# Kernel tuning notes

Hardware: AMD Instinct MI355X
Metric: run time of the kernel (lower is better)

## Reference

```python
import jax, jax.numpy as jnp
import numpy as np

D_MODEL = 1024
H = 16
D_K = D_MODEL // H


def setup_inputs() -> dict:
    key = jax.random.key(0)
    ks = jax.random.split(key, 9)
    B, S = 4, 2048
    s = 1.0 / np.sqrt(D_MODEL)
    return {
        "query": jax.random.normal(ks[0], (B, S, D_MODEL), jnp.float32),
        "key_": jax.random.normal(ks[1], (B, S, D_MODEL), jnp.float32),
        "value": jax.random.normal(ks[2], (B, S, D_MODEL), jnp.float32),
        "Wq": jax.random.normal(ks[3], (D_MODEL, D_MODEL), jnp.float32) * s,
        "bq": jnp.zeros((D_MODEL,), jnp.float32),
        "Wk": jax.random.normal(ks[4], (D_MODEL, D_MODEL), jnp.float32) * s,
        "bk": jnp.zeros((D_MODEL,), jnp.float32),
        "Wv": jax.random.normal(ks[5], (D_MODEL, D_MODEL), jnp.float32) * s,
        "bv": jnp.zeros((D_MODEL,), jnp.float32),
    }


def reference(query, key_, value, Wq, bq, Wk, bk, Wv, bv):
    B, S, _ = query.shape
    # separate Q/K/V projections (torch Linear: x @ W.T + b)
    q = (query @ Wq.T + bq).reshape(B, S, H, D_K).transpose(0, 2, 1, 3)  # [B,H,S,Dk]
    k = (key_ @ Wk.T + bk).reshape(B, S, H, D_K).transpose(0, 2, 1, 3)
    v = (value @ Wv.T + bv).reshape(B, S, H, D_K).transpose(0, 2, 1, 3)
    # naive scaled dot-product attention (full [B,H,S,S] scores)
    scores = jnp.einsum("bhqd,bhkd->bhqk", q, k) / jnp.sqrt(jnp.float32(D_K))
    attn = jax.nn.softmax(scores, axis=-1)
    out = jnp.einsum("bhqk,bhkd->bhqd", attn, v)  # [B,H,S,Dk]
    # merge heads; NOTE: original forward never applies self.wo
    return out.transpose(0, 2, 1, 3).reshape(B, S, D_MODEL)
```

## Files before the change

kernel.cpp:

```cpp
#include <hip/hip_runtime.h>
#include <math.h>

#define DEVI __device__ __forceinline__

typedef short bf16x8 __attribute__((ext_vector_type(8)));
typedef float f32x4 __attribute__((ext_vector_type(4)));
typedef float f32x16 __attribute__((ext_vector_type(16)));
typedef unsigned short u16x8 __attribute__((ext_vector_type(8)));
typedef unsigned short u16x4 __attribute__((ext_vector_type(4)));
typedef unsigned int u32x2 __attribute__((ext_vector_type(2)));
typedef int i32x4 __attribute__((ext_vector_type(4)));

static constexpr int S_LEN = 2048;
static constexpr int DMODEL = 1024;
static constexpr int NH = 16;
static constexpr int DK = 64;

DEVI unsigned short f2bf(float f) {
  unsigned int u = __builtin_bit_cast(unsigned int, f);
  u = u + 0x7fffu + ((u >> 16) & 1u);
  return (unsigned short)(u >> 16);
}
DEVI unsigned cvtpk(float lo, float hi) {
  unsigned d;
  asm("v_cvt_pk_bf16_f32 %0, %1, %2" : "=v"(d) : "v"(lo), "v"(hi));
  return d;
}
DEVI float bitf(unsigned u) { return __builtin_bit_cast(float, u); }
DEVI unsigned bitu(float f) { return __builtin_bit_cast(unsigned, f); }

#if __has_builtin(__builtin_amdgcn_exp2f)
DEVI float fexp2(float x) { return __builtin_amdgcn_exp2f(x); }
#else
DEVI float fexp2(float x) { return __expf(x * 0.69314718055994531f); }
#endif

typedef __attribute__((address_space(3))) unsigned int lds_u32;
typedef __attribute__((address_space(1))) const unsigned int glb_u32;

DEVI void gload16(const void* g, void* lds) {
  __builtin_amdgcn_global_load_lds((glb_u32*)reinterpret_cast<uintptr_t>(g),
                                   (lds_u32*)reinterpret_cast<uintptr_t>(lds),
                                   16, 0, 0);
}

__global__ __launch_bounds__(256) void cvt_f32_bf16(const float* __restrict__ in,
                                                    unsigned short* __restrict__ out,
                                                    int n8) {
  int i = blockIdx.x * 256 + threadIdx.x;
  if (i >= n8) return;
  const float4* p = (const float4*)in + (size_t)i * 2;
  float4 a = p[0], b = p[1];
  u16x8 o;
  o[0] = f2bf(a.x); o[1] = f2bf(a.y); o[2] = f2bf(a.z); o[3] = f2bf(a.w);
  o[4] = f2bf(b.x); o[5] = f2bf(b.y); o[6] = f2bf(b.z); o[7] = f2bf(b.w);
  *((u16x8*)out + i) = o;
}

template <int VT>
__global__ __launch_bounds__(256) void proj_gemm(const unsigned short* __restrict__ A,
                                                 const unsigned short* __restrict__ W,
                                                 const float* __restrict__ bias,
                                                 unsigned short* __restrict__ C,
                                                 float scale) {
  __shared__ unsigned short As[128 * 32];
  __shared__ unsigned short Bs[128 * 32];
  const int m0 = blockIdx.x * 128, n0 = blockIdx.y * 128;
  const int tid = threadIdx.x, wid = tid >> 6, lane = tid & 63;
  const int l15 = lane & 15, lg = lane >> 4;
  const int mb = (wid >> 1) * 64, nb = (wid & 1) * 64;

  f32x4 acc[4][4] = {};

  for (int kk = 0; kk < 32; ++kk) {
    const int k0 = kk * 32;
#pragma unroll
    for (int i = 0; i < 2; ++i) {
      const int jbase = (wid * 2 + i) * 1024;
      const int o = jbase + lane * 16;
      const int row = o >> 6, inner = o & 63;
      gload16((const char*)A + (size_t)(m0 + row) * 2048 + k0 * 2 + inner,
              (char*)As + jbase);
      gload16((const char*)W + (size_t)(n0 + row) * 2048 + k0 * 2 + inner,
              (char*)Bs + jbase);
    }
    __syncthreads();

    bf16x8 af[4], bfr[4];
#pragma unroll
    for (int ms = 0; ms < 4; ++ms)
      af[ms] = *(const bf16x8*)&As[(mb + ms * 16 + l15) * 32 + lg * 8];
#pragma unroll
    for (int ns = 0; ns < 4; ++ns)
      bfr[ns] = *(const bf16x8*)&Bs[(nb + ns * 16 + l15) * 32 + lg * 8];
#pragma unroll
    for (int ms = 0; ms < 4; ++ms)
#pragma unroll
      for (int ns = 0; ns < 4; ++ns)
        acc[ms][ns] = __builtin_amdgcn_mfma_f32_16x16x32_bf16(af[ms], bfr[ns],
                                                              acc[ms][ns], 0, 0, 0);
    __syncthreads();
  }

#pragma unroll
  for (int ms = 0; ms < 4; ++ms) {
#pragma unroll
    for (int ns = 0; ns < 4; ++ns) {
      const int n = n0 + nb + ns * 16 + l15;
      const float bv = bias[n];
      const int mbase = m0 + mb + ms * 16 + lg * 4;
      if (VT) {
        u16x4 pk4;
#pragma unroll
        for (int r = 0; r < 4; ++r) pk4[r] = f2bf((acc[ms][ns][r] + bv) * scale);
        const size_t oi =
            (((size_t)(mbase >> 11) * NH + (n >> 6)) * DK + (n & 63)) * S_LEN + (mbase & 2047);
        *(u16x4*)&C[oi] = pk4;
      } else {
#pragma unroll
        for (int r = 0; r < 4; ++r) {
          const int m = mbase + r;
          const size_t oi =
              (((size_t)(m >> 11) * NH + (n >> 6)) * S_LEN + (m & 2047)) * DK + (n & 63);
          C[oi] = f2bf((acc[ms][ns][r] + bv) * scale);
        }
      }
    }
  }
}

__global__ __launch_bounds__(256) void attn_fwd(const unsigned short* __restrict__ Q,
                                                const unsigned short* __restrict__ K,
                                                const unsigned short* __restrict__ Vt,
                                                float* __restrict__ Out) {
  const int id = blockIdx.x;
  const int o = (id & 7) * 128 + (id >> 3);
  const int qt = o & 15, bh = o >> 4;

  const unsigned short* Qb = Q + (size_t)bh * S_LEN * DK;
  const char* Kb = (const char*)(K + (size_t)bh * S_LEN * DK);
  const char* Vb = (const char*)(Vt + (size_t)bh * DK * S_LEN);
  float* Ob = Out + (size_t)(bh >> 4) * S_LEN * DMODEL + (bh & 15) * DK;

  __shared__ unsigned short Ks[2][64][64];
  __shared__ unsigned short Vs[2][64][64];

  const int tid = threadIdx.x, w = tid >> 6, lane = tid & 63;
  const int l31 = lane & 31, hi = lane >> 5;
  const int q0 = qt * 128 + w * 32;
  const int swzr = (l31 & 7) ^ (((l31 >> 3) & 3) << 1);

  const int s8 = lane >> 3;
  int cs[2];
#pragma unroll
  for (int i = 0; i < 2; ++i)
    cs[i] = (((lane & 7) ^ s8) ^ (((w * 2 + i) & 3) << 1)) * 16;

  bf16x8 qf[4];
  {
    const unsigned short* qp = Qb + (size_t)(q0 + l31) * DK + hi * 8;
#pragma unroll
    for (int d = 0; d < 4; ++d) qf[d] = *(const bf16x8*)(qp + d * 16);
  }

  f32x16 oacc0 = {}, oacc1 = {};
  float m_r = 0.f;
  float lacc[4] = {0.f, 0.f, 0.f, 0.f};

  const int krow0 = w * 16;

#pragma unroll
  for (int i = 0; i < 2; ++i) {
    gload16(Kb + (size_t)(krow0 + i * 8 + s8) * 128 + cs[i],
            (char*)&Ks[0][krow0 + i * 8][0]);
    gload16(Vb + (size_t)(krow0 + i * 8 + s8) * 4096 + cs[i],
            (char*)&Vs[0][krow0 + i * 8][0]);
  }
  asm volatile("s_waitcnt vmcnt(0)" ::: "memory");
  __syncthreads();

  int buf = 0;
  for (int it = 0; it < 32; ++it) {
    if (it < 31) {
      const int j0 = (it + 1) * 64;
#pragma unroll
      for (int i = 0; i < 2; ++i) {
        gload16(Kb + (size_t)(j0 + krow0 + i * 8 + s8) * 128 + cs[i],
                (char*)&Ks[buf ^ 1][krow0 + i * 8][0]);
        gload16(Vb + (size_t)(krow0 + i * 8 + s8) * 4096 + j0 * 2 + cs[i],
                (char*)&Vs[buf ^ 1][krow0 + i * 8][0]);
      }
    }
    const char* ksb = (const char*)&Ks[buf][0][0];
    const char* vsb = (const char*)&Vs[buf][0][0];

    f32x16 sac0 = {}, sac1 = {};
#pragma unroll
    for (int d = 0; d < 4; ++d) {
      bf16x8 k0 = *(const bf16x8*)(ksb + (size_t)(l31)*128 + (((2 * d + hi) ^ swzr) * 16));
      bf16x8 k1 = *(const bf16x8*)(ksb + (size_t)(32 + l31) * 128 + (((2 * d + hi) ^ swzr) * 16));
      sac0 = __builtin_amdgcn_mfma_f32_32x32x16_bf16(k0, qf[d], sac0, 0, 0, 0);
      sac1 = __builtin_amdgcn_mfma_f32_32x32x16_bf16(k1, qf[d], sac1, 0, 0, 0);
    }

    float mx[8];
#pragma unroll
    for (int i = 0; i < 8; ++i)
      mx[i] = fmaxf(fmaxf(sac0[2 * i], sac0[2 * i + 1]),
                    fmaxf(sac1[2 * i], sac1[2 * i + 1]));
    float pmA = fmaxf(fmaxf(mx[0], mx[1]), fmaxf(mx[2], mx[3]));
    float pmB = fmaxf(fmaxf(mx[4], mx[5]), fmaxf(mx[6], mx[7]));
    float pm = fmaxf(pmA, pmB);

#pragma unroll
    for (int r = 0; r < 16; ++r) {
      const float p = fexp2(sac0[r] - m_r);
      sac0[r] = p;
      lacc[r & 3] += p;
    }
#pragma unroll
    for (int r = 0; r < 16; ++r) {
      const float p = fexp2(sac1[r] - m_r);
      sac1[r] = p;
      lacc[r & 3] += p;
    }
    {
      u32x2 t = __builtin_amdgcn_permlane32_swap(bitu(pm), bitu(pm), false, false);
      pm = fmaxf(bitf(t[0]), bitf(t[1]));
    }

    if (__any(pm - m_r > 8.f)) {
      const float mn = fmaxf(m_r, pm);
      const float esc = fexp2(m_r - mn);
      m_r = mn;
#pragma unroll
      for (int i = 0; i < 4; ++i) lacc[i] *= esc;
#pragma unroll
      for (int r = 0; r < 16; ++r) { sac0[r] *= esc; sac1[r] *= esc; }
#pragma unroll
      for (int r = 0; r < 16; ++r) {
        const float er = __shfl(esc, ((r & 3) + 8 * (r >> 2)) + hi * 4);
        oacc0[r] *= er;
        oacc1[r] *= er;
      }
    }

#pragma unroll
    for (int jb = 0; jb < 2; ++jb) {
      const f32x16& e = jb ? sac1 : sac0;
      unsigned pk[8];
#pragma unroll
      for (int m = 0; m < 8; ++m) pk[m] = cvtpk(e[2 * m], e[2 * m + 1]);
#pragma unroll
      for (int ks = 0; ks < 2; ++ks) {
        u32x2 s02 = __builtin_amdgcn_permlane32_swap(pk[4 * ks], pk[4 * ks + 2], false, false);
        u32x2 s13 = __builtin_amdgcn_permlane32_swap(pk[4 * ks + 1], pk[4 * ks + 3], false, false);
        i32x4 paw = {(int)s02[0], (int)s13[0], (int)s02[1], (int)s13[1]};
        bf16x8 pa = __builtin_bit_cast(bf16x8, paw);
        const int vslot = ((4 * jb + 2 * ks + hi) ^ swzr) * 16;
        bf16x8 v0 = *(const bf16x8*)(vsb + (size_t)(l31)*128 + vslot);
        bf16x8 v1 = *(const bf16x8*)(vsb + (size_t)(32 + l31) * 128 + vslot);
        oacc0 = __builtin_amdgcn_mfma_f32_32x32x16_bf16(pa, v0, oacc0, 0, 0, 0);
        oacc1 = __builtin_amdgcn_mfma_f32_32x32x16_bf16(pa, v1, oacc1, 0, 0, 0);
      }
    }

    asm volatile("s_waitcnt vmcnt(0)" ::: "memory");
    __syncthreads();
    buf ^= 1;
  }

  float l_r = (lacc[0] + lacc[1]) + (lacc[2] + lacc[3]);
  {
    u32x2 t = __builtin_amdgcn_permlane32_swap(bitu(l_r), bitu(l_r), false, false);
    l_r = bitf(t[0]) + bitf(t[1]);
  }
  const float linv = 1.f / l_r;
#pragma unroll
  for (int r = 0; r < 16; ++r) {
    const int cr = (r & 3) + 8 * (r >> 2);
    const float li = __shfl(linv, cr + hi * 4);
    const int qg = q0 + cr + 4 * hi;
    float* op = Ob + (size_t)qg * DMODEL;
    op[l31] = oacc0[r] * li;
    op[32 + l31] = oacc1[r] * li;
  }
}

extern "C" void kernel_launch(void* const* d_in, const int* in_sizes, int n_in,
                              void* d_out, int out_size, void* d_ws, size_t ws_size,
                              hipStream_t stream) {
  (void)in_sizes; (void)n_in; (void)out_size; (void)ws_size;
  const float* q_in = (const float*)d_in[0];
  const float* k_in = (const float*)d_in[1];
  const float* v_in = (const float*)d_in[2];
  const float* Wq = (const float*)d_in[3];
  const float* bq = (const float*)d_in[4];
  const float* Wk = (const float*)d_in[5];
  const float* bk = (const float*)d_in[6];
  const float* Wv = (const float*)d_in[7];
  const float* bv = (const float*)d_in[8];
  float* out = (float*)d_out;

  char* ws = (char*)d_ws;
  unsigned short* Xbf = (unsigned short*)(ws);
  unsigned short* Wbf = (unsigned short*)(ws + 16777216);
  unsigned short* Qh  = (unsigned short*)(ws + 18874368);
  unsigned short* Kh  = Qh + 8388608;
  unsigned short* Vt  = Kh + 8388608;

  const int nX8 = (4 * S_LEN * DMODEL) / 8;
  const int nW8 = (DMODEL * DMODEL) / 8;
  const dim3 gGemm(64, 8);

  const float qscale = 0.125f * 1.44269504088896340736f;

  cvt_f32_bf16<<<4096, 256, 0, stream>>>(q_in, Xbf, nX8);
  cvt_f32_bf16<<<512, 256, 0, stream>>>(Wq, Wbf, nW8);
  proj_gemm<0><<<gGemm, 256, 0, stream>>>(Xbf, Wbf, bq, Qh, qscale);

  cvt_f32_bf16<<<4096, 256, 0, stream>>>(k_in, Xbf, nX8);
  cvt_f32_bf16<<<512, 256, 0, stream>>>(Wk, Wbf, nW8);
  proj_gemm<0><<<gGemm, 256, 0, stream>>>(Xbf, Wbf, bk, Kh, 1.0f);

  cvt_f32_bf16<<<4096, 256, 0, stream>>>(v_in, Xbf, nX8);
  cvt_f32_bf16<<<512, 256, 0, stream>>>(Wv, Wbf, nW8);
  proj_gemm<1><<<gGemm, 256, 0, stream>>>(Xbf, Wbf, bv, Vt, 1.0f);

  attn_fwd<<<1024, 256, 0, stream>>>(Qh, Kh, Vt, out);
}
```

Baseline: 210.7 us.

## Fuse fp32-to-bf16 activation conversion into projection GEMM and skip max subtraction initially

The projection GEMM now loads fp32 activations straight into LDS and converts them to bf16 while building MFMA fragments. This removes the three separate activation conversion kernels and their bf16 round trip through global memory. In exchange the GEMM reads twice as many bytes per A tile, uses more LDS and does conversion ALU work in its inner loop. The attention kernel also adds a branch that skips subtracting the running max until the first rescale, which is a minor ALU saving.

```diff
diff --git a/kernel.cpp b/kernel.cpp
--- a/kernel.cpp
+++ b/kernel.cpp
@@ -58,12 +58,12 @@
 }
 
 template <int VT>
-__global__ __launch_bounds__(256) void proj_gemm(const unsigned short* __restrict__ A,
+__global__ __launch_bounds__(256) void proj_gemm(const float* __restrict__ A,
                                                  const unsigned short* __restrict__ W,
                                                  const float* __restrict__ bias,
                                                  unsigned short* __restrict__ C,
                                                  float scale) {
-  __shared__ unsigned short As[128 * 32];
+  __shared__ float Af[2][128][16];
   __shared__ unsigned short Bs[128 * 32];
   const int m0 = blockIdx.x * 128, n0 = blockIdx.y * 128;
   const int tid = threadIdx.x, wid = tid >> 6, lane = tid & 63;
@@ -73,23 +73,35 @@
   f32x4 acc[4][4] = {};
 
   for (int kk = 0; kk < 32; ++kk) {
-    const int k0 = kk * 32;
+    const int k0b = kk * 128;
+#pragma unroll
+    for (int i = 0; i < 4; ++i) {
+      const int jb = (wid * 4 + i) * 1024;
+      const int h = jb >> 13;
+      const int o = (jb & 8191) + lane * 16;
+      const int row = o >> 6, inner = o & 63;
+      gload16((const char*)A + (size_t)(m0 + row) * 4096 + k0b + h * 64 + inner,
+              (char*)Af + jb);
+    }
 #pragma unroll
     for (int i = 0; i < 2; ++i) {
-      const int jbase = (wid * 2 + i) * 1024;
-      const int o = jbase + lane * 16;
+      const int jb = (wid * 2 + i) * 1024;
+      const int o = jb + lane * 16;
       const int row = o >> 6, inner = o & 63;
-      gload16((const char*)A + (size_t)(m0 + row) * 2048 + k0 * 2 + inner,
-              (char*)As + jbase);
-      gload16((const char*)W + (size_t)(n0 + row) * 2048 + k0 * 2 + inner,
-              (char*)Bs + jbase);
+      gload16((const char*)W + (size_t)(n0 + row) * 2048 + kk * 64 + inner,
+              (char*)Bs + jb);
     }
     __syncthreads();
 
     bf16x8 af[4], bfr[4];
 #pragma unroll
-    for (int ms = 0; ms < 4; ++ms)
-      af[ms] = *(const bf16x8*)&As[(mb + ms * 16 + l15) * 32 + lg * 8];
+    for (int ms = 0; ms < 4; ++ms) {
+      const float* ap = &Af[lg >> 1][mb + ms * 16 + l15][(lg & 1) * 8];
+      f32x4 a0 = *(const f32x4*)ap, a1 = *(const f32x4*)(ap + 4);
+      i32x4 wv = {(int)cvtpk(a0[0], a0[1]), (int)cvtpk(a0[2], a0[3]),
+                  (int)cvtpk(a1[0], a1[1]), (int)cvtpk(a1[2], a1[3])};
+      af[ms] = __builtin_bit_cast(bf16x8, wv);
+    }
 #pragma unroll
     for (int ns = 0; ns < 4; ++ns)
       bfr[ns] = *(const bf16x8*)&Bs[(nb + ns * 16 + l15) * 32 + lg * 8];
@@ -165,6 +177,7 @@
 
   f32x16 oacc0 = {}, oacc1 = {};
   float m_r = 0.f;
+  bool virgin = true;
   float lacc[4] = {0.f, 0.f, 0.f, 0.f};
 
   const int krow0 = w * 16;
@@ -212,17 +225,32 @@
     float pmB = fmaxf(fmaxf(mx[4], mx[5]), fmaxf(mx[6], mx[7]));
     float pm = fmaxf(pmA, pmB);
 
-#pragma unroll
-    for (int r = 0; r < 16; ++r) {
-      const float p = fexp2(sac0[r] - m_r);
-      sac0[r] = p;
-      lacc[r & 3] += p;
-    }
-#pragma unroll
-    for (int r = 0; r < 16; ++r) {
-      const float p = fexp2(sac1[r] - m_r);
-      sac1[r] = p;
-      lacc[r & 3] += p;
+    if (virgin) {
+#pragma unroll
+      for (int r = 0; r < 16; ++r) {
+        const float p = fexp2(sac0[r]);
+        sac0[r] = p;
+        lacc[r & 3] += p;
+      }
+#pragma unroll
+      for (int r = 0; r < 16; ++r) {
+        const float p = fexp2(sac1[r]);
+        sac1[r] = p;
+        lacc[r & 3] += p;
+      }
+    } else {
+#pragma unroll
+      for (int r = 0; r < 16; ++r) {
+        const float p = fexp2(sac0[r] - m_r);
+        sac0[r] = p;
+        lacc[r & 3] += p;
+      }
+#pragma unroll
+      for (int r = 0; r < 16; ++r) {
+        const float p = fexp2(sac1[r] - m_r);
+        sac1[r] = p;
+        lacc[r & 3] += p;
+      }
     }
     {
       u32x2 t = __builtin_amdgcn_permlane32_swap(bitu(pm), bitu(pm), false, false);
@@ -233,6 +261,7 @@
       const float mn = fmaxf(m_r, pm);
       const float esc = fexp2(m_r - mn);
       m_r = mn;
+      virgin = false;
 #pragma unroll
       for (int i = 0; i < 4; ++i) lacc[i] *= esc;
 #pragma unroll
@@ -303,29 +332,24 @@
   float* out = (float*)d_out;
 
   char* ws = (char*)d_ws;
-  unsigned short* Xbf = (unsigned short*)(ws);
   unsigned short* Wbf = (unsigned short*)(ws + 16777216);
   unsigned short* Qh  = (unsigned short*)(ws + 18874368);
   unsigned short* Kh  = Qh + 8388608;
   unsigned short* Vt  = Kh + 8388608;
 
-  const int nX8 = (4 * S_LEN * DMODEL) / 8;
   const int nW8 = (DMODEL * DMODEL) / 8;
   const dim3 gGemm(64, 8);
 
   const float qscale = 0.125f * 1.44269504088896340736f;
 
-  cvt_f32_bf16<<<4096, 256, 0, stream>>>(q_in, Xbf, nX8);
   cvt_f32_bf16<<<512, 256, 0, stream>>>(Wq, Wbf, nW8);
-  proj_gemm<0><<<gGemm, 256, 0, stream>>>(Xbf, Wbf, bq, Qh, qscale);
-
-  cvt_f32_bf16<<<4096, 256, 0, stream>>>(k_in, Xbf, nX8);
+  proj_gemm<0><<<gGemm, 256, 0, stream>>>(q_in, Wbf, bq, Qh, qscale);
+
   cvt_f32_bf16<<<512, 256, 0, stream>>>(Wk, Wbf, nW8);
-  proj_gemm<0><<<gGemm, 256, 0, stream>>>(Xbf, Wbf, bk, Kh, 1.0f);
-
-  cvt_f32_bf16<<<4096, 256, 0, stream>>>(v_in, Xbf, nX8);
+  proj_gemm<0><<<gGemm, 256, 0, stream>>>(k_in, Wbf, bk, Kh, 1.0f);
+
   cvt_f32_bf16<<<512, 256, 0, stream>>>(Wv, Wbf, nW8);
-  proj_gemm<1><<<gGemm, 256, 0, stream>>>(Xbf, Wbf, bv, Vt, 1.0f);
+  proj_gemm<1><<<gGemm, 256, 0, stream>>>(v_in, Wbf, bv, Vt, 1.0f);
 
   attn_fwd<<<1024, 256, 0, stream>>>(Qh, Kh, Vt, out);
 }
```

Result: no change. 211.4 us (+0.3%).
